# Kernel optimization log

Measured on AMD Instinct MI355X. Metric: run time of the kernel, lower is better.

Reference implementation:

```python
import jax, jax.numpy as jnp
import numpy as np

NUM_ENVS = 16384
NUM_AGENTS = 16
IN_DIM = 128
GCN_H = 64
RNN_H = 64
E_PER_GRAPH = 128
N_FEAT = 4   # num_individual_actions_features
N_CAT = 8    # num_action_categories
OUT_DIM = NUM_AGENTS * N_FEAT * N_CAT


def setup_inputs() -> dict:
    key = jax.random.key(0)
    ks = jax.random.split(key, 10)
    x = jax.random.normal(ks[0], (NUM_ENVS, NUM_AGENTS, IN_DIM), dtype=jnp.float32)
    edge_index = jax.random.randint(ks[1], (NUM_ENVS, 2, E_PER_GRAPH), 0, NUM_AGENTS, dtype=jnp.int64)
    prev_h = jax.random.normal(ks[2], (NUM_ENVS, NUM_AGENTS, RNN_H), dtype=jnp.float32)
    s = 0.05
    W_gcn = jax.random.normal(ks[3], (IN_DIM, GCN_H), dtype=jnp.float32) * s
    b_gcn = jnp.zeros((GCN_H,), dtype=jnp.float32)
    W_ih = jax.random.normal(ks[4], (3 * RNN_H, GCN_H), dtype=jnp.float32) * s
    W_hh = jax.random.normal(ks[5], (3 * RNN_H, RNN_H), dtype=jnp.float32) * s
    b_ih = jax.random.normal(ks[6], (3 * RNN_H,), dtype=jnp.float32) * s
    b_hh = jax.random.normal(ks[7], (3 * RNN_H,), dtype=jnp.float32) * s
    W_lin = jax.random.normal(ks[8], (OUT_DIM, NUM_AGENTS * RNN_H), dtype=jnp.float32) * s
    b_lin = jax.random.normal(ks[9], (OUT_DIM,), dtype=jnp.float32) * s
    return {"x": x, "edge_index": edge_index, "prev_rnn_hidden_state": prev_h,
            "W_gcn": W_gcn, "b_gcn": b_gcn, "W_ih": W_ih, "W_hh": W_hh,
            "b_ih": b_ih, "b_hh": b_hh, "W_lin": W_lin, "b_lin": b_lin}


def _forward(x, edge_index, prev_h, W_gcn, b_gcn, W_ih, W_hh, b_ih, b_hh, W_lin, b_lin):
    num_envs = x.shape[0]
    N = num_envs * NUM_AGENTS  # flattened node count
    x_flat = x.reshape(N, IN_DIM)

    # block-offset trick: one big disconnected graph
    offsets = (jnp.arange(num_envs, dtype=edge_index.dtype) * NUM_AGENTS)[:, None, None]  # [env,1,1]
    ei = (edge_index + offsets).reshape(num_envs, 2, -1)  # offsets broadcast over [env,2,E]
    row = ei[:, 0, :].reshape(-1)  # source nodes, [env*E]
    col = ei[:, 1, :].reshape(-1)  # target nodes

    # GCNConv: xw = x @ W; add self-loops; sym-normalize; scatter-add to targets
    xw = x_flat @ W_gcn  # [N, GCN_H]
    ones_e = jnp.ones(row.shape[0], dtype=x.dtype)
    deg = jnp.ones((N,), dtype=x.dtype) + jax.ops.segment_sum(ones_e, col, num_segments=N)
    dinv = jax.lax.rsqrt(deg)
    norm = dinv[row] * dinv[col]  # [env*E]
    msg = norm[:, None] * xw[row]  # gather + scale
    agg = jnp.zeros_like(xw).at[col].add(msg)
    agg = agg + xw / deg[:, None]  # self-loop term: 1/deg * xw
    gcn_out = agg + b_gcn  # [N, GCN_H]

    # single-step GRU (torch gate order: r, z, n)
    h = prev_h.reshape(N, RNN_H)
    gx = gcn_out @ W_ih.T + b_ih  # [N, 3H]
    gh = h @ W_hh.T + b_hh
    rx, zx, nx = jnp.split(gx, 3, axis=-1)
    rh, zh, nh = jnp.split(gh, 3, axis=-1)
    r = jax.nn.sigmoid(rx + rh)
    z = jax.nn.sigmoid(zx + zh)
    n = jnp.tanh(nx + r * nh)
    h_new = (1.0 - z) * n + z * h  # [N, H]

    flat = h_new.reshape(num_envs, NUM_AGENTS * RNN_H)
    logits = flat @ W_lin.T + b_lin  # [env, OUT_DIM]
    next_h = h_new.reshape(num_envs, NUM_AGENTS, RNN_H)
    return logits, next_h


def reference(x, edge_index, prev_rnn_hidden_state, W_gcn, b_gcn, W_ih, W_hh, b_ih, b_hh, W_lin, b_lin):
    return _forward(x, edge_index, prev_rnn_hidden_state, W_gcn, b_gcn, W_ih, W_hh, b_ih, b_hh, W_lin, b_lin)
```

## Files before the change

### kernel.cpp

```cpp
#include <hip/hip_runtime.h>
#include <math.h>

namespace {

constexpr int NUM_ENVS = 16384;
constexpr int OUT_DIM = 512;
constexpr int FLAT = 1024;

typedef float floatx4 __attribute__((ext_vector_type(4)));
typedef short shortx8 __attribute__((ext_vector_type(8)));

__device__ __forceinline__ float fast_sigmoid(float v) {
    const float e = __builtin_amdgcn_exp2f(-v * 1.44269504088896340736f);
    return __builtin_amdgcn_rcpf(1.0f + e);
}
__device__ __forceinline__ float fast_tanh(float v) {
    const float e = __builtin_amdgcn_exp2f(v * 2.88539008177792681472f);
    return 1.0f - 2.0f * __builtin_amdgcn_rcpf(1.0f + e);
}
__device__ __forceinline__ unsigned short f2bf(float f) {
    unsigned int u = __float_as_uint(f);
    u = (u + 0x7FFFu + ((u >> 16) & 1u)) >> 16;
    return (unsigned short)u;
}
__device__ __forceinline__ float bf2f(unsigned short s) {
    return __uint_as_float(((unsigned int)s) << 16);
}
__device__ __forceinline__ shortx8 pack8(const float4& f0, const float4& f1) {
    shortx8 o;
    o[0] = (short)f2bf(f0.x); o[1] = (short)f2bf(f0.y);
    o[2] = (short)f2bf(f0.z); o[3] = (short)f2bf(f0.w);
    o[4] = (short)f2bf(f1.x); o[5] = (short)f2bf(f1.y);
    o[6] = (short)f2bf(f1.z); o[7] = (short)f2bf(f1.w);
    return o;
}

constexpr int WS_FLAG = 0;
constexpr int WS_WGF  = 64;
constexpr int WS_WCF  = WS_WGF + 4096;
constexpr int WS_WLB  = WS_WCF + 12288;
constexpr int WS_GB   = WS_WLB + 262144;

__global__ void prep_kernel(const int* __restrict__ edges_i32,
                            const float* __restrict__ Wg,
                            const float* __restrict__ Wih,
                            const float* __restrict__ Whh,
                            const float* __restrict__ Wlin,
                            float* __restrict__ ws) {
    if (blockIdx.x == 0) {
        __shared__ int any_nonzero;
        if (threadIdx.x == 0) any_nonzero = 0;
        __syncthreads();
        if (threadIdx.x < 128 && edges_i32[2 * threadIdx.x + 1] != 0)
            atomicOr(&any_nonzero, 1);
        __syncthreads();
        if (threadIdx.x == 0) ((int*)ws)[WS_FLAG] = (any_nonzero == 0) ? 1 : 0;
        return;
    }
    const int t = ((int)blockIdx.x - 1) * 256 + (int)threadIdx.x;
    if (t < 8192) {
        const int jj = t & 7, lane = (t >> 3) & 63, slot = t >> 9;
        const int nt = slot >> 2, ks = slot & 3;
        const int n = nt * 16 + (lane & 15);
        const int k = ks * 32 + ((lane >> 4) & 3) * 8 + jj;
        ((unsigned short*)(ws + WS_WGF))[t] = f2bf(Wg[k * 64 + n]);
    } else if (t < 32768) {
        const int u = t - 8192;
        const int jj = u & 7, lane = (u >> 3) & 63, slot = u >> 9;
        const int q8 = ((lane >> 4) & 3) * 8 + jj;
        float val;
        if (slot < 16) {
            const int nt = slot >> 2, ks = slot & 3;
            const int n = nt * 16 + (lane & 15);
            const int k = ks * 32 + q8;
            val = (k < 64) ? Wih[n * 64 + k] : Whh[n * 64 + (k - 64)];
        } else if (slot < 32) {
            const int s = slot - 16, nt = s >> 2, ks = s & 3;
            const int n = 64 + nt * 16 + (lane & 15);
            const int k = ks * 32 + q8;
            val = (k < 64) ? Wih[n * 64 + k] : Whh[n * 64 + (k - 64)];
        } else if (slot < 40) {
            const int s = slot - 32, nt = s >> 1, ks = s & 1;
            const int n = 128 + nt * 16 + (lane & 15);
            val = Wih[n * 64 + ks * 32 + q8];
        } else {
            const int s = slot - 40, nt = s >> 1, ks = s & 1;
            const int n = 128 + nt * 16 + (lane & 15);
            val = Whh[n * 64 + ks * 32 + q8];
        }
        ((unsigned short*)(ws + WS_WCF))[u] = f2bf(val);
    } else if (t < 32768 + 524288) {
        const int u = t - 32768;
        ((unsigned short*)(ws + WS_WLB))[u] = f2bf(Wlin[u]);
    }
}

__global__ __launch_bounds__(256, 3) void fused_gcn_gru_kernel(
    const float* __restrict__ x,
    const void*  __restrict__ edges,
    const unsigned short* __restrict__ WgF,
    const float* __restrict__ bg,
    const float* __restrict__ h_prev,
    const unsigned short* __restrict__ WcF,
    const float* __restrict__ bih,
    const float* __restrict__ bhh,
    float* __restrict__ next_h,
    unsigned short* __restrict__ hb,
    const int* __restrict__ flag64)
{
    const int b = blockIdx.x;
    const int tid = threadIdx.x;
    const int lane = tid & 63;
    const int w = tid >> 6;

    __shared__ float xw_s[64 * 68];
    __shared__ unsigned short A_s[64 * 136];
    __shared__ int rc_s[512];
    __shared__ float adj_s[4][16][17];
    __shared__ int deg_s[4][16];
    __shared__ float dinv_s[4][16];
    __shared__ float invdeg_s[4][16];

    const int ar = w * 16 + (lane & 15);
    const int aq = (lane >> 4) & 3;

    float4 xf[4][2];
    #pragma unroll
    for (int ks = 0; ks < 4; ++ks) {
        const float4* p = (const float4*)(x + ((size_t)b * 64 + ar) * 128 + ks * 32 + aq * 8);
        xf[ks][0] = p[0];
        xf[ks][1] = p[1];
    }

    {
        float* ap = &adj_s[0][0][0];
        for (int i = tid; i < 4 * 16 * 17; i += 256) ap[i] = 0.0f;
        if (tid < 64) deg_s[tid >> 4][tid & 15] = 0;
    }
    {
        const int r = tid >> 2, q = tid & 3;
        const float4* src = (const float4*)(h_prev + ((size_t)b * 64 + r) * 64 + q * 16);
        const float4 f0 = src[0], f1 = src[1], f2 = src[2], f3 = src[3];
        unsigned short* dp = &A_s[r * 136 + 64 + q * 16];
        *(shortx8*)dp = pack8(f0, f1);
        *(shortx8*)(dp + 8) = pack8(f2, f3);
    }
    const bool is64 = (*flag64 != 0);
    #pragma unroll
    for (int t = 0; t < 2; ++t) {
        const int e = tid + 256 * t;
        const int el = e >> 7, idx = e & 127;
        const size_t base = ((size_t)b * 4 + el) * 256;
        int rv, cv;
        if (is64) {
            rv = (int)((const long long*)edges)[base + idx];
            cv = (int)((const long long*)edges)[base + 128 + idx];
        } else {
            rv = ((const int*)edges)[base + idx];
            cv = ((const int*)edges)[base + 128 + idx];
        }
        rc_s[e] = rv | (cv << 8);
    }
    __syncthreads();

    #pragma unroll
    for (int t = 0; t < 2; ++t) {
        const int e = tid + 256 * t;
        atomicAdd(&deg_s[e >> 7][(rc_s[e] >> 8) & 15], 1);
    }

    shortx8 afr[4];
    #pragma unroll
    for (int ks = 0; ks < 4; ++ks) afr[ks] = pack8(xf[ks][0], xf[ks][1]);
    floatx4 acc[4];
    #pragma unroll
    for (int nt = 0; nt < 4; ++nt) acc[nt] = (floatx4)(0.0f);
    #pragma unroll
    for (int nt = 0; nt < 4; ++nt) {
        #pragma unroll
        for (int ks = 0; ks < 4; ++ks) {
            const shortx8 bfr = *(const shortx8*)&WgF[((nt * 4 + ks) * 64 + lane) * 8];
            acc[nt] = __builtin_amdgcn_mfma_f32_16x16x32_bf16(afr[ks], bfr, acc[nt], 0, 0, 0);
        }
    }
    __syncthreads();

    if (tid < 64) {
        const float d = 1.0f + (float)deg_s[tid >> 4][tid & 15];
        dinv_s[tid >> 4][tid & 15] = rsqrtf(d);
        invdeg_s[tid >> 4][tid & 15] = 1.0f / d;
    }
    #pragma unroll
    for (int nt = 0; nt < 4; ++nt)
        #pragma unroll
        for (int i = 0; i < 4; ++i)
            xw_s[(w * 16 + aq * 4 + i) * 68 + nt * 16 + (lane & 15)] = acc[nt][i];
    __syncthreads();

    #pragma unroll
    for (int t = 0; t < 2; ++t) {
        const int e = tid + 256 * t;
        const int el = e >> 7;
        const int r = rc_s[e] & 15, c = (rc_s[e] >> 8) & 15;
        atomicAdd(&adj_s[el][c][r], dinv_s[el][r] * dinv_s[el][c]);
    }
    if (tid < 64)
        atomicAdd(&adj_s[tid >> 4][tid & 15][tid & 15], invdeg_s[tid >> 4][tid & 15]);
    __syncthreads();

    {
        const int ro = tid >> 2, q = tid & 3;
        const int el = ro >> 4, cl = ro & 15;
        float accs[16];
        #pragma unroll
        for (int m = 0; m < 16; ++m) accs[m] = 0.0f;
        for (int r16 = 0; r16 < 16; ++r16) {
            const float a = adj_s[el][cl][r16];
            const float4* xr = (const float4*)&xw_s[(el * 16 + r16) * 68 + q * 16];
            #pragma unroll
            for (int jq = 0; jq < 4; ++jq) {
                const float4 v = xr[jq];
                accs[4 * jq + 0] += a * v.x;
                accs[4 * jq + 1] += a * v.y;
                accs[4 * jq + 2] += a * v.z;
                accs[4 * jq + 3] += a * v.w;
            }
        }
        unsigned short* dst = &A_s[ro * 136 + q * 16];
        shortx8 o0, o1;
        #pragma unroll
        for (int m = 0; m < 8; ++m) o0[m] = (short)f2bf(accs[m] + bg[q * 16 + m]);
        #pragma unroll
        for (int m = 0; m < 8; ++m) o1[m] = (short)f2bf(accs[8 + m] + bg[q * 16 + 8 + m]);
        *(shortx8*)dst = o0;
        *(shortx8*)(dst + 8) = o1;
    }
    __syncthreads();

    shortx8 gfr[4];
    #pragma unroll
    for (int ks = 0; ks < 4; ++ks)
        gfr[ks] = *(const shortx8*)&A_s[ar * 136 + ks * 32 + aq * 8];
    floatx4 aR[4], aZ[4], aNX[4], aNH[4];
    #pragma unroll
    for (int nt = 0; nt < 4; ++nt) {
        aR[nt] = (floatx4)(0.0f); aZ[nt] = (floatx4)(0.0f);
        aNX[nt] = (floatx4)(0.0f); aNH[nt] = (floatx4)(0.0f);
    }
    #pragma unroll
    for (int nt = 0; nt < 4; ++nt) {
        #pragma unroll
        for (int ks = 0; ks < 4; ++ks) {
            const shortx8 bfr = *(const shortx8*)&WcF[((nt * 4 + ks) * 64 + lane) * 8];
            aR[nt] = __builtin_amdgcn_mfma_f32_16x16x32_bf16(gfr[ks], bfr, aR[nt], 0, 0, 0);
        }
        #pragma unroll
        for (int ks = 0; ks < 4; ++ks) {
            const shortx8 bfr = *(const shortx8*)&WcF[((16 + nt * 4 + ks) * 64 + lane) * 8];
            aZ[nt] = __builtin_amdgcn_mfma_f32_16x16x32_bf16(gfr[ks], bfr, aZ[nt], 0, 0, 0);
        }
        #pragma unroll
        for (int ks = 0; ks < 2; ++ks) {
            const shortx8 bfr = *(const shortx8*)&WcF[((32 + nt * 2 + ks) * 64 + lane) * 8];
            aNX[nt] = __builtin_amdgcn_mfma_f32_16x16x32_bf16(gfr[ks], bfr, aNX[nt], 0, 0, 0);
        }
        #pragma unroll
        for (int ks = 0; ks < 2; ++ks) {
            const shortx8 bfr = *(const shortx8*)&WcF[((40 + nt * 2 + ks) * 64 + lane) * 8];
            aNH[nt] = __builtin_amdgcn_mfma_f32_16x16x32_bf16(gfr[ks + 2], bfr, aNH[nt], 0, 0, 0);
        }
    }

    const int cl2 = lane & 15;
    const int rq = (lane >> 4) & 3;
    #pragma unroll
    for (int tp = 0; tp < 4; ++tp) {
        const int f = tp * 16 + cl2;
        const float br = bih[f] + bhh[f];
        const float bz = bih[64 + f] + bhh[64 + f];
        const float bnx = bih[128 + f];
        const float bnh = bhh[128 + f];
        #pragma unroll
        for (int i = 0; i < 4; ++i) {
            const int rl = w * 16 + rq * 4 + i;
            const size_t row = (size_t)b * 64 + rl;
            const float hp = bf2f(A_s[rl * 136 + 64 + f]);
            const float r = fast_sigmoid(aR[tp][i] + br);
            const float z = fast_sigmoid(aZ[tp][i] + bz);
            const float n = fast_tanh(aNX[tp][i] + bnx + r * (aNH[tp][i] + bnh));
            const float hv = (1.0f - z) * n + z * hp;
            next_h[row * 64 + f] = hv;
            hb[row * 64 + f] = f2bf(hv);
        }
    }
}

__global__ __launch_bounds__(256, 4) void logits_mfma_kernel(
    const unsigned short* __restrict__ A,
    const unsigned short* __restrict__ B,
    const float* __restrict__ bias,
    float* __restrict__ C)
{
    __shared__ __align__(16) unsigned short As[128 * 64];
    __shared__ __align__(16) unsigned short Bs[128 * 64];

    const int tid = threadIdx.x;
    const int lane = tid & 63;
    const int wave = tid >> 6;
    const int wr = wave >> 1;
    const int wc = wave & 1;
    const int m0 = blockIdx.y * 128;
    const int n0 = blockIdx.x * 128;
    const int lr = tid >> 3;
    const int lk = tid & 7;

    floatx4 acc[4][4];
    #pragma unroll
    for (int i = 0; i < 4; ++i)
        #pragma unroll
        for (int jn = 0; jn < 4; ++jn)
            acc[i][jn] = (floatx4)(0.0f);

    for (int kt = 0; kt < 16; ++kt) {
        const int k0 = kt * 64;
        __syncthreads();
        #pragma unroll
        for (int i = 0; i < 4; ++i) {
            const int r = lr + 32 * i;
            const uint4 va = *(const uint4*)&A[(size_t)(m0 + r) * FLAT + k0 + lk * 8];
            *(uint4*)&As[r * 64 + ((lk ^ (r & 7)) * 8)] = va;
            const uint4 vb = *(const uint4*)&B[(size_t)(n0 + r) * FLAT + k0 + lk * 8];
            *(uint4*)&Bs[r * 64 + ((lk ^ (r & 7)) * 8)] = vb;
        }
        __syncthreads();
        #pragma unroll
        for (int s = 0; s < 2; ++s) {
            const int kg = s * 4 + (lane >> 4);
            const int sw = (kg ^ (lane & 7)) * 8;
            shortx8 af[4], bf[4];
            #pragma unroll
            for (int t = 0; t < 4; ++t) {
                af[t] = *(const shortx8*)&As[(wr * 64 + t * 16 + (lane & 15)) * 64 + sw];
                bf[t] = *(const shortx8*)&Bs[(wc * 64 + t * 16 + (lane & 15)) * 64 + sw];
            }
            #pragma unroll
            for (int mt = 0; mt < 4; ++mt)
                #pragma unroll
                for (int nt = 0; nt < 4; ++nt)
                    acc[mt][nt] = __builtin_amdgcn_mfma_f32_16x16x32_bf16(
                        af[mt], bf[nt], acc[mt][nt], 0, 0, 0);
        }
    }

    const int col_l = lane & 15;
    const int rg = lane >> 4;
    #pragma unroll
    for (int nt = 0; nt < 4; ++nt) {
        const int col = n0 + wc * 64 + nt * 16 + col_l;
        const float bv = bias[col];
        #pragma unroll
        for (int mt = 0; mt < 4; ++mt) {
            const int row = m0 + wr * 64 + mt * 16 + rg * 4;
            #pragma unroll
            for (int i = 0; i < 4; ++i) {
                C[(size_t)(row + i) * OUT_DIM + col] = acc[mt][nt][i] + bv;
            }
        }
    }
}

}

extern "C" void kernel_launch(void* const* d_in, const int* in_sizes, int n_in,
                              void* d_out, int out_size, void* d_ws, size_t ws_size,
                              hipStream_t stream) {
    const float* x    = (const float*)d_in[0];
    const void*  ei   = d_in[1];
    const float* h0   = (const float*)d_in[2];
    const float* Wg   = (const float*)d_in[3];
    const float* bg   = (const float*)d_in[4];
    const float* Wih  = (const float*)d_in[5];
    const float* Whh  = (const float*)d_in[6];
    const float* bih  = (const float*)d_in[7];
    const float* bhh  = (const float*)d_in[8];
    const float* Wlin = (const float*)d_in[9];
    const float* blin = (const float*)d_in[10];

    float* out = (float*)d_out;
    float* logits = out;
    float* next_h = out + (size_t)NUM_ENVS * OUT_DIM;

    float* wsf = (float*)d_ws;
    int* flag = (int*)(wsf + WS_FLAG);
    unsigned short* WgF = (unsigned short*)(wsf + WS_WGF);
    unsigned short* WcF = (unsigned short*)(wsf + WS_WCF);
    unsigned short* Wlb = (unsigned short*)(wsf + WS_WLB);
    unsigned short* gb  = (unsigned short*)(wsf + WS_GB);

    prep_kernel<<<2177, 256, 0, stream>>>((const int*)ei, Wg, Wih, Whh, Wlin, wsf);
    fused_gcn_gru_kernel<<<4096, 256, 0, stream>>>(x, ei, WgF, bg, h0, WcF, bih, bhh,
                                                   next_h, gb, flag);
    dim3 g2(OUT_DIM / 128, NUM_ENVS / 128);
    logits_mfma_kernel<<<g2, 256, 0, stream>>>(gb, Wlb, blin, logits);
}
```

Before: 396.7 us.

## Split fused GCN+GRU kernel into per-env GCN kernel and LDS-staged GRU GEMM

The fused kernel, which handled four environments per 256-thread block, is split into two kernels. The first is a 64-thread-per-environment GCN kernel that writes bf16 GCN output to a workspace buffer. The second is a GRU GEMM kernel that stages the packed GRU weights in LDS once per block and loops over four 16-row tiles per wave. This is meant to cut per-block weight traffic from global memory and to reduce shared-memory pressure in the GCN stage. The cost is an extra kernel launch and a round trip of the intermediate GCN activations through global memory. The GRU output now overwrites the same gb buffer in place, and h_prev is read from global twice.

```diff
diff --git a/kernel.cpp b/kernel.cpp
--- a/kernel.cpp
+++ b/kernel.cpp
@@ -22,9 +22,6 @@
     unsigned int u = __float_as_uint(f);
     u = (u + 0x7FFFu + ((u >> 16) & 1u)) >> 16;
     return (unsigned short)u;
-}
-__device__ __forceinline__ float bf2f(unsigned short s) {
-    return __uint_as_float(((unsigned int)s) << 16);
 }
 __device__ __forceinline__ shortx8 pack8(const float4& f0, const float4& f1) {
     shortx8 o;
@@ -95,79 +92,62 @@
     }
 }
 
-__global__ __launch_bounds__(256, 3) void fused_gcn_gru_kernel(
+__global__ __launch_bounds__(64, 4) void gcn_env_kernel(
     const float* __restrict__ x,
     const void*  __restrict__ edges,
     const unsigned short* __restrict__ WgF,
     const float* __restrict__ bg,
-    const float* __restrict__ h_prev,
-    const unsigned short* __restrict__ WcF,
-    const float* __restrict__ bih,
-    const float* __restrict__ bhh,
-    float* __restrict__ next_h,
-    unsigned short* __restrict__ hb,
+    unsigned short* __restrict__ gcn,
     const int* __restrict__ flag64)
 {
-    const int b = blockIdx.x;
-    const int tid = threadIdx.x;
-    const int lane = tid & 63;
-    const int w = tid >> 6;
-
-    __shared__ float xw_s[64 * 68];
-    __shared__ unsigned short A_s[64 * 136];
-    __shared__ int rc_s[512];
-    __shared__ float adj_s[4][16][17];
-    __shared__ int deg_s[4][16];
-    __shared__ float dinv_s[4][16];
-    __shared__ float invdeg_s[4][16];
-
-    const int ar = w * 16 + (lane & 15);
-    const int aq = (lane >> 4) & 3;
+    const int env = blockIdx.x;
+    const int lane = threadIdx.x;
+
+    __shared__ float xw_s[16 * 68];
+    __shared__ float adj_s[16][17];
+    __shared__ int   deg_s[16];
+    __shared__ float dinv_s[16];
+    __shared__ float invdeg_s[16];
+
+    const int ar = lane & 15;
+    const int aq = lane >> 4;
 
     float4 xf[4][2];
     #pragma unroll
     for (int ks = 0; ks < 4; ++ks) {
-        const float4* p = (const float4*)(x + ((size_t)b * 64 + ar) * 128 + ks * 32 + aq * 8);
+        const float4* p = (const float4*)(x + ((size_t)env * 16 + ar) * 128 + ks * 32 + aq * 8);
         xf[ks][0] = p[0];
         xf[ks][1] = p[1];
     }
 
+    const bool is64 = (*flag64 != 0);
+    int rv[2], cv[2];
+    const size_t ebase = (size_t)env * 256;
+    #pragma unroll
+    for (int t = 0; t < 2; ++t) {
+        const int idx = lane + 64 * t;
+        if (is64) {
+            rv[t] = (int)((const long long*)edges)[ebase + idx];
+            cv[t] = (int)((const long long*)edges)[ebase + 128 + idx];
+        } else {
+            rv[t] = ((const int*)edges)[ebase + idx];
+            cv[t] = ((const int*)edges)[ebase + 128 + idx];
+        }
+    }
+
+    if (lane < 16) deg_s[lane] = 0;
     {
-        float* ap = &adj_s[0][0][0];
-        for (int i = tid; i < 4 * 16 * 17; i += 256) ap[i] = 0.0f;
-        if (tid < 64) deg_s[tid >> 4][tid & 15] = 0;
-    }
-    {
-        const int r = tid >> 2, q = tid & 3;
-        const float4* src = (const float4*)(h_prev + ((size_t)b * 64 + r) * 64 + q * 16);
-        const float4 f0 = src[0], f1 = src[1], f2 = src[2], f3 = src[3];
-        unsigned short* dp = &A_s[r * 136 + 64 + q * 16];
-        *(shortx8*)dp = pack8(f0, f1);
-        *(shortx8*)(dp + 8) = pack8(f2, f3);
-    }
-    const bool is64 = (*flag64 != 0);
-    #pragma unroll
-    for (int t = 0; t < 2; ++t) {
-        const int e = tid + 256 * t;
-        const int el = e >> 7, idx = e & 127;
-        const size_t base = ((size_t)b * 4 + el) * 256;
-        int rv, cv;
-        if (is64) {
-            rv = (int)((const long long*)edges)[base + idx];
-            cv = (int)((const long long*)edges)[base + 128 + idx];
-        } else {
-            rv = ((const int*)edges)[base + idx];
-            cv = ((const int*)edges)[base + 128 + idx];
-        }
-        rc_s[e] = rv | (cv << 8);
+        float* ap = &adj_s[0][0];
+        #pragma unroll
+        for (int i = 0; i < 5; ++i) {
+            const int j = lane + 64 * i;
+            if (j < 272) ap[j] = 0.0f;
+        }
     }
     __syncthreads();
 
     #pragma unroll
-    for (int t = 0; t < 2; ++t) {
-        const int e = tid + 256 * t;
-        atomicAdd(&deg_s[e >> 7][(rc_s[e] >> 8) & 15], 1);
-    }
+    for (int t = 0; t < 2; ++t) atomicAdd(&deg_s[cv[t]], 1);
 
     shortx8 afr[4];
     #pragma unroll
@@ -185,38 +165,33 @@
     }
     __syncthreads();
 
-    if (tid < 64) {
-        const float d = 1.0f + (float)deg_s[tid >> 4][tid & 15];
-        dinv_s[tid >> 4][tid & 15] = rsqrtf(d);
-        invdeg_s[tid >> 4][tid & 15] = 1.0f / d;
+    if (lane < 16) {
+        const float d = 1.0f + (float)deg_s[lane];
+        dinv_s[lane] = rsqrtf(d);
+        invdeg_s[lane] = 1.0f / d;
     }
     #pragma unroll
     for (int nt = 0; nt < 4; ++nt)
         #pragma unroll
         for (int i = 0; i < 4; ++i)
-            xw_s[(w * 16 + aq * 4 + i) * 68 + nt * 16 + (lane & 15)] = acc[nt][i];
+            xw_s[(aq * 4 + i) * 68 + nt * 16 + ar] = acc[nt][i];
     __syncthreads();
 
     #pragma unroll
-    for (int t = 0; t < 2; ++t) {
-        const int e = tid + 256 * t;
-        const int el = e >> 7;
-        const int r = rc_s[e] & 15, c = (rc_s[e] >> 8) & 15;
-        atomicAdd(&adj_s[el][c][r], dinv_s[el][r] * dinv_s[el][c]);
-    }
-    if (tid < 64)
-        atomicAdd(&adj_s[tid >> 4][tid & 15][tid & 15], invdeg_s[tid >> 4][tid & 15]);
+    for (int t = 0; t < 2; ++t)
+        atomicAdd(&adj_s[cv[t]][rv[t]], dinv_s[rv[t]] * dinv_s[cv[t]]);
+    if (lane < 16)
+        atomicAdd(&adj_s[lane][lane], invdeg_s[lane]);
     __syncthreads();
 
     {
-        const int ro = tid >> 2, q = tid & 3;
-        const int el = ro >> 4, cl = ro & 15;
+        const int cl = lane >> 2, q = lane & 3;
         float accs[16];
         #pragma unroll
         for (int m = 0; m < 16; ++m) accs[m] = 0.0f;
         for (int r16 = 0; r16 < 16; ++r16) {
-            const float a = adj_s[el][cl][r16];
-            const float4* xr = (const float4*)&xw_s[(el * 16 + r16) * 68 + q * 16];
+            const float a = adj_s[cl][r16];
+            const float4* xr = (const float4*)&xw_s[r16 * 68 + q * 16];
             #pragma unroll
             for (int jq = 0; jq < 4; ++jq) {
                 const float4 v = xr[jq];
@@ -226,7 +201,7 @@
                 accs[4 * jq + 3] += a * v.w;
             }
         }
-        unsigned short* dst = &A_s[ro * 136 + q * 16];
+        unsigned short* dst = gcn + ((size_t)env * 16 + cl) * 64 + q * 16;
         shortx8 o0, o1;
         #pragma unroll
         for (int m = 0; m < 8; ++m) o0[m] = (short)f2bf(accs[m] + bg[q * 16 + m]);
@@ -235,62 +210,105 @@
         *(shortx8*)dst = o0;
         *(shortx8*)(dst + 8) = o1;
     }
-    __syncthreads();
-
-    shortx8 gfr[4];
-    #pragma unroll
-    for (int ks = 0; ks < 4; ++ks)
-        gfr[ks] = *(const shortx8*)&A_s[ar * 136 + ks * 32 + aq * 8];
-    floatx4 aR[4], aZ[4], aNX[4], aNH[4];
-    #pragma unroll
-    for (int nt = 0; nt < 4; ++nt) {
-        aR[nt] = (floatx4)(0.0f); aZ[nt] = (floatx4)(0.0f);
-        aNX[nt] = (floatx4)(0.0f); aNH[nt] = (floatx4)(0.0f);
-    }
-    #pragma unroll
-    for (int nt = 0; nt < 4; ++nt) {
-        #pragma unroll
-        for (int ks = 0; ks < 4; ++ks) {
-            const shortx8 bfr = *(const shortx8*)&WcF[((nt * 4 + ks) * 64 + lane) * 8];
-            aR[nt] = __builtin_amdgcn_mfma_f32_16x16x32_bf16(gfr[ks], bfr, aR[nt], 0, 0, 0);
-        }
-        #pragma unroll
-        for (int ks = 0; ks < 4; ++ks) {
-            const shortx8 bfr = *(const shortx8*)&WcF[((16 + nt * 4 + ks) * 64 + lane) * 8];
-            aZ[nt] = __builtin_amdgcn_mfma_f32_16x16x32_bf16(gfr[ks], bfr, aZ[nt], 0, 0, 0);
-        }
-        #pragma unroll
-        for (int ks = 0; ks < 2; ++ks) {
-            const shortx8 bfr = *(const shortx8*)&WcF[((32 + nt * 2 + ks) * 64 + lane) * 8];
-            aNX[nt] = __builtin_amdgcn_mfma_f32_16x16x32_bf16(gfr[ks], bfr, aNX[nt], 0, 0, 0);
-        }
-        #pragma unroll
-        for (int ks = 0; ks < 2; ++ks) {
-            const shortx8 bfr = *(const shortx8*)&WcF[((40 + nt * 2 + ks) * 64 + lane) * 8];
-            aNH[nt] = __builtin_amdgcn_mfma_f32_16x16x32_bf16(gfr[ks + 2], bfr, aNH[nt], 0, 0, 0);
-        }
+}
+
+__global__ __launch_bounds__(256, 3) void gru_gemm_kernel(
+    unsigned short* __restrict__ gb,
+    const float* __restrict__ h_prev,
+    const unsigned short* __restrict__ WcF,
+    const float* __restrict__ bih,
+    const float* __restrict__ bhh,
+    float* __restrict__ next_h)
+{
+    const int tid = threadIdx.x;
+    const int lane = tid & 63;
+    const int w = tid >> 6;
+
+    __shared__ unsigned short W_s[48 * 64 * 8];
+
+    {
+        const uint4* src = (const uint4*)WcF;
+        uint4* dst = (uint4*)W_s;
+        #pragma unroll
+        for (int jq = 0; jq < 12; ++jq) dst[tid + 256 * jq] = src[tid + 256 * jq];
     }
 
     const int cl2 = lane & 15;
-    const int rq = (lane >> 4) & 3;
+    const int rq = lane >> 4;
+    float brv[4], bzv[4], bnxv[4], bnhv[4];
     #pragma unroll
     for (int tp = 0; tp < 4; ++tp) {
         const int f = tp * 16 + cl2;
-        const float br = bih[f] + bhh[f];
-        const float bz = bih[64 + f] + bhh[64 + f];
-        const float bnx = bih[128 + f];
-        const float bnh = bhh[128 + f];
-        #pragma unroll
-        for (int i = 0; i < 4; ++i) {
-            const int rl = w * 16 + rq * 4 + i;
-            const size_t row = (size_t)b * 64 + rl;
-            const float hp = bf2f(A_s[rl * 136 + 64 + f]);
-            const float r = fast_sigmoid(aR[tp][i] + br);
-            const float z = fast_sigmoid(aZ[tp][i] + bz);
-            const float n = fast_tanh(aNX[tp][i] + bnx + r * (aNH[tp][i] + bnh));
-            const float hv = (1.0f - z) * n + z * hp;
-            next_h[row * 64 + f] = hv;
-            hb[row * 64 + f] = f2bf(hv);
+        brv[tp] = bih[f] + bhh[f];
+        bzv[tp] = bih[64 + f] + bhh[64 + f];
+        bnxv[tp] = bih[128 + f];
+        bnhv[tp] = bhh[128 + f];
+    }
+    __syncthreads();
+
+    const int rl = lane & 15;
+    const int aq = rq;
+
+    #pragma unroll 1
+    for (int t = 0; t < 4; ++t) {
+        const size_t base = (size_t)blockIdx.x * 256 + (size_t)w * 64 + t * 16;
+
+        shortx8 afr[4];
+        const unsigned short* gp = gb + (base + rl) * 64;
+        afr[0] = *(const shortx8*)(gp + aq * 8);
+        afr[1] = *(const shortx8*)(gp + 32 + aq * 8);
+        const float* hp4 = h_prev + (base + rl) * 64;
+        {
+            const float4* pa = (const float4*)(hp4 + aq * 8);
+            afr[2] = pack8(pa[0], pa[1]);
+            const float4* pb = (const float4*)(hp4 + 32 + aq * 8);
+            afr[3] = pack8(pb[0], pb[1]);
+        }
+
+        floatx4 aR[4], aZ[4], aNX[4], aNH[4];
+        #pragma unroll
+        for (int nt = 0; nt < 4; ++nt) {
+            aR[nt] = (floatx4)(0.0f); aZ[nt] = (floatx4)(0.0f);
+            aNX[nt] = (floatx4)(0.0f); aNH[nt] = (floatx4)(0.0f);
+        }
+        #pragma unroll
+        for (int nt = 0; nt < 4; ++nt) {
+            #pragma unroll
+            for (int ks = 0; ks < 4; ++ks) {
+                const shortx8 bfr = *(const shortx8*)&W_s[((nt * 4 + ks) * 64 + lane) * 8];
+                aR[nt] = __builtin_amdgcn_mfma_f32_16x16x32_bf16(afr[ks], bfr, aR[nt], 0, 0, 0);
+            }
+            #pragma unroll
+            for (int ks = 0; ks < 4; ++ks) {
+                const shortx8 bfr = *(const shortx8*)&W_s[((16 + nt * 4 + ks) * 64 + lane) * 8];
+                aZ[nt] = __builtin_amdgcn_mfma_f32_16x16x32_bf16(afr[ks], bfr, aZ[nt], 0, 0, 0);
+            }
+            #pragma unroll
+            for (int ks = 0; ks < 2; ++ks) {
+                const shortx8 bfr = *(const shortx8*)&W_s[((32 + nt * 2 + ks) * 64 + lane) * 8];
+                aNX[nt] = __builtin_amdgcn_mfma_f32_16x16x32_bf16(afr[ks], bfr, aNX[nt], 0, 0, 0);
+            }
+            #pragma unroll
+            for (int ks = 0; ks < 2; ++ks) {
+                const shortx8 bfr = *(const shortx8*)&W_s[((40 + nt * 2 + ks) * 64 + lane) * 8];
+                aNH[nt] = __builtin_amdgcn_mfma_f32_16x16x32_bf16(afr[ks + 2], bfr, aNH[nt], 0, 0, 0);
+            }
+        }
+
+        #pragma unroll
+        for (int tp = 0; tp < 4; ++tp) {
+            const int f = tp * 16 + cl2;
+            #pragma unroll
+            for (int i = 0; i < 4; ++i) {
+                const size_t row = base + rq * 4 + i;
+                const float hp = h_prev[row * 64 + f];
+                const float r = fast_sigmoid(aR[tp][i] + brv[tp]);
+                const float z = fast_sigmoid(aZ[tp][i] + bzv[tp]);
+                const float n = fast_tanh(aNX[tp][i] + bnxv[tp] + r * (aNH[tp][i] + bnhv[tp]));
+                const float hv = (1.0f - z) * n + z * hp;
+                next_h[row * 64 + f] = hv;
+                gb[row * 64 + f] = f2bf(hv);
+            }
         }
     }
 }
@@ -398,8 +416,8 @@
     unsigned short* gb  = (unsigned short*)(wsf + WS_GB);
 
     prep_kernel<<<2177, 256, 0, stream>>>((const int*)ei, Wg, Wih, Whh, Wlin, wsf);
-    fused_gcn_gru_kernel<<<4096, 256, 0, stream>>>(x, ei, WgF, bg, h0, WcF, bih, bhh,
-                                                   next_h, gb, flag);
+    gcn_env_kernel<<<NUM_ENVS, 64, 0, stream>>>(x, ei, WgF, bg, gb, flag);
+    gru_gemm_kernel<<<1024, 256, 0, stream>>>(gb, h0, WcF, bih, bhh, next_h);
     dim3 g2(OUT_DIM / 128, NUM_ENVS / 128);
     logits_mfma_kernel<<<g2, 256, 0, stream>>>(gb, Wlb, blin, logits);
 }
```

Result: slower. 535.3 us (+35.0%).

## Double-buffer logits GEMM tiles and keep h_prev fragments in registers

Applied to the files above, without the earlier changes.

The logits GEMM now double-buffers its LDS tiles. The next K-tile is prefetched into registers while MFMAs run on the current buffer, which halves the barriers per iteration, at the cost of twice the LDS and a lower occupancy hint (2 blocks). The fused GCN/GRU kernel stops staging h_prev as bf16 in shared memory. It loads the MFMA fragments for h directly into registers and rereads h_prev in fp32 from global memory for the GRU blend, which shrinks A_s and raises the occupancy hint to 4. Using fp32 h_prev in the blend is also slightly more accurate.

```diff
diff --git a/kernel.cpp b/kernel.cpp
--- a/kernel.cpp
+++ b/kernel.cpp
@@ -22,9 +22,6 @@
     unsigned int u = __float_as_uint(f);
     u = (u + 0x7FFFu + ((u >> 16) & 1u)) >> 16;
     return (unsigned short)u;
-}
-__device__ __forceinline__ float bf2f(unsigned short s) {
-    return __uint_as_float(((unsigned int)s) << 16);
 }
 __device__ __forceinline__ shortx8 pack8(const float4& f0, const float4& f1) {
     shortx8 o;
@@ -95,7 +92,7 @@
     }
 }
 
-__global__ __launch_bounds__(256, 3) void fused_gcn_gru_kernel(
+__global__ __launch_bounds__(256, 4) void fused_gcn_gru_kernel(
     const float* __restrict__ x,
     const void*  __restrict__ edges,
     const unsigned short* __restrict__ WgF,
@@ -114,7 +111,7 @@
     const int w = tid >> 6;
 
     __shared__ float xw_s[64 * 68];
-    __shared__ unsigned short A_s[64 * 136];
+    __shared__ unsigned short A_s[64 * 72];
     __shared__ int rc_s[512];
     __shared__ float adj_s[4][16][17];
     __shared__ int deg_s[4][16];
@@ -131,19 +128,19 @@
         xf[ks][0] = p[0];
         xf[ks][1] = p[1];
     }
+    shortx8 hfr2, hfr3;
+    {
+        const float* hp4 = h_prev + ((size_t)b * 64 + ar) * 64;
+        const float4* pa = (const float4*)(hp4 + aq * 8);
+        hfr2 = pack8(pa[0], pa[1]);
+        const float4* pb = (const float4*)(hp4 + 32 + aq * 8);
+        hfr3 = pack8(pb[0], pb[1]);
+    }
 
     {
         float* ap = &adj_s[0][0][0];
         for (int i = tid; i < 4 * 16 * 17; i += 256) ap[i] = 0.0f;
         if (tid < 64) deg_s[tid >> 4][tid & 15] = 0;
-    }
-    {
-        const int r = tid >> 2, q = tid & 3;
-        const float4* src = (const float4*)(h_prev + ((size_t)b * 64 + r) * 64 + q * 16);
-        const float4 f0 = src[0], f1 = src[1], f2 = src[2], f3 = src[3];
-        unsigned short* dp = &A_s[r * 136 + 64 + q * 16];
-        *(shortx8*)dp = pack8(f0, f1);
-        *(shortx8*)(dp + 8) = pack8(f2, f3);
     }
     const bool is64 = (*flag64 != 0);
     #pragma unroll
@@ -226,7 +223,7 @@
                 accs[4 * jq + 3] += a * v.w;
             }
         }
-        unsigned short* dst = &A_s[ro * 136 + q * 16];
+        unsigned short* dst = &A_s[ro * 72 + q * 16];
         shortx8 o0, o1;
         #pragma unroll
         for (int m = 0; m < 8; ++m) o0[m] = (short)f2bf(accs[m] + bg[q * 16 + m]);
@@ -238,9 +235,10 @@
     __syncthreads();
 
     shortx8 gfr[4];
-    #pragma unroll
-    for (int ks = 0; ks < 4; ++ks)
-        gfr[ks] = *(const shortx8*)&A_s[ar * 136 + ks * 32 + aq * 8];
+    gfr[0] = *(const shortx8*)&A_s[ar * 72 + aq * 8];
+    gfr[1] = *(const shortx8*)&A_s[ar * 72 + 32 + aq * 8];
+    gfr[2] = hfr2;
+    gfr[3] = hfr3;
     floatx4 aR[4], aZ[4], aNX[4], aNH[4];
     #pragma unroll
     for (int nt = 0; nt < 4; ++nt) {
@@ -284,7 +282,7 @@
         for (int i = 0; i < 4; ++i) {
             const int rl = w * 16 + rq * 4 + i;
             const size_t row = (size_t)b * 64 + rl;
-            const float hp = bf2f(A_s[rl * 136 + 64 + f]);
+            const float hp = h_prev[row * 64 + f];
             const float r = fast_sigmoid(aR[tp][i] + br);
             const float z = fast_sigmoid(aZ[tp][i] + bz);
             const float n = fast_tanh(aNX[tp][i] + bnx + r * (aNH[tp][i] + bnh));
@@ -295,14 +293,14 @@
     }
 }
 
-__global__ __launch_bounds__(256, 4) void logits_mfma_kernel(
+__global__ __launch_bounds__(256, 2) void logits_mfma_kernel(
     const unsigned short* __restrict__ A,
     const unsigned short* __restrict__ B,
     const float* __restrict__ bias,
     float* __restrict__ C)
 {
-    __shared__ __align__(16) unsigned short As[128 * 64];
-    __shared__ __align__(16) unsigned short Bs[128 * 64];
+    __shared__ __align__(16) unsigned short As[2][128 * 64];
+    __shared__ __align__(16) unsigned short Bs[2][128 * 64];
 
     const int tid = threadIdx.x;
     const int lane = tid & 63;
@@ -321,18 +319,33 @@
         for (int jn = 0; jn < 4; ++jn)
             acc[i][jn] = (floatx4)(0.0f);
 
-    for (int kt = 0; kt < 16; ++kt) {
+    uint4 ra[4], rb[4];
+    auto load_tile = [&](int kt) {
         const int k0 = kt * 64;
-        __syncthreads();
         #pragma unroll
         for (int i = 0; i < 4; ++i) {
             const int r = lr + 32 * i;
-            const uint4 va = *(const uint4*)&A[(size_t)(m0 + r) * FLAT + k0 + lk * 8];
-            *(uint4*)&As[r * 64 + ((lk ^ (r & 7)) * 8)] = va;
-            const uint4 vb = *(const uint4*)&B[(size_t)(n0 + r) * FLAT + k0 + lk * 8];
-            *(uint4*)&Bs[r * 64 + ((lk ^ (r & 7)) * 8)] = vb;
-        }
-        __syncthreads();
+            ra[i] = *(const uint4*)&A[(size_t)(m0 + r) * FLAT + k0 + lk * 8];
+            rb[i] = *(const uint4*)&B[(size_t)(n0 + r) * FLAT + k0 + lk * 8];
+        }
+    };
+    auto write_tile = [&](int buf) {
+        #pragma unroll
+        for (int i = 0; i < 4; ++i) {
+            const int r = lr + 32 * i;
+            *(uint4*)&As[buf][r * 64 + ((lk ^ (r & 7)) * 8)] = ra[i];
+            *(uint4*)&Bs[buf][r * 64 + ((lk ^ (r & 7)) * 8)] = rb[i];
+        }
+    };
+
+    load_tile(0);
+    write_tile(0);
+    __syncthreads();
+
+    #pragma unroll 2
+    for (int kt = 0; kt < 16; ++kt) {
+        const int cur = kt & 1;
+        if (kt < 15) load_tile(kt + 1);
         #pragma unroll
         for (int s = 0; s < 2; ++s) {
             const int kg = s * 4 + (lane >> 4);
@@ -340,8 +353,8 @@
             shortx8 af[4], bf[4];
             #pragma unroll
             for (int t = 0; t < 4; ++t) {
-                af[t] = *(const shortx8*)&As[(wr * 64 + t * 16 + (lane & 15)) * 64 + sw];
-                bf[t] = *(const shortx8*)&Bs[(wc * 64 + t * 16 + (lane & 15)) * 64 + sw];
+                af[t] = *(const shortx8*)&As[cur][(wr * 64 + t * 16 + (lane & 15)) * 64 + sw];
+                bf[t] = *(const shortx8*)&Bs[cur][(wc * 64 + t * 16 + (lane & 15)) * 64 + sw];
             }
             #pragma unroll
             for (int mt = 0; mt < 4; ++mt)
@@ -349,6 +362,10 @@
                 for (int nt = 0; nt < 4; ++nt)
                     acc[mt][nt] = __builtin_amdgcn_mfma_f32_16x16x32_bf16(
                         af[mt], bf[nt], acc[mt][nt], 0, 0, 0);
+        }
+        if (kt < 15) {
+            write_tile(cur ^ 1);
+            __syncthreads();
         }
     }
 
```

Result: faster. 388.2 us (-2.1%).
